# Optimization experiments

Measured on AMD Instinct MI355X. Metric: run time of the kernel, lower is better.

## Reference

```python
import jax, jax.numpy as jnp
import numpy as np

B, N, C_IN, C_OUT, NUM_TYPES = 4, 4096, 128, 64, 5
TEMP = 1.0  # self.temp is undefined in the source; use 1.0


def setup_inputs() -> dict:
    key = jax.random.key(0)
    ks = jax.random.split(key, 9)
    bound_p = np.sqrt(6.0 / (C_IN + C_OUT))
    bound_k = np.sqrt(6.0 / (C_OUT + 1))
    return {
        "node_rep": jax.random.normal(ks[0], (B, N, C_IN), dtype=jnp.float32),
        "adj_matrix": jax.random.uniform(ks[1], (N, N), dtype=jnp.float32),
        "node_type": jax.random.randint(ks[2], (N,), 0, NUM_TYPES),
        "proj_W": jax.random.uniform(ks[3], (C_OUT, C_IN), minval=-bound_p, maxval=bound_p, dtype=jnp.float32),
        "proj_b": jnp.zeros((C_OUT,), dtype=jnp.float32),
        "k_W": jax.random.uniform(ks[4], (NUM_TYPES, C_OUT), minval=-bound_k, maxval=bound_k, dtype=jnp.float32),
        "k_b": jnp.zeros((NUM_TYPES,), dtype=jnp.float32),
        "v_W": jax.random.uniform(ks[5], (NUM_TYPES, C_OUT), minval=-bound_k, maxval=bound_k, dtype=jnp.float32),
        "v_b": jnp.zeros((NUM_TYPES,), dtype=jnp.float32),
    }


def reference(node_rep, adj_matrix, node_type, proj_W, proj_b, k_W, k_b, v_W, v_b):
    # projection: [B,N,c_in] -> [B,N,c_out]
    h = jnp.einsum('bnc,oc->bno', node_rep, proj_W) + proj_b
    # per-type scalar scores stacked: [B,N,num_types]
    ks = jnp.einsum('bno,to->bnt', h, k_W) + k_b
    vs = jnp.einsum('bno,to->bnt', h, v_W) + v_b
    # gather score of each node's own type -> [B,N,1]
    idx = jnp.broadcast_to(node_type[None, :, None], (h.shape[0], h.shape[1], 1))
    f1 = jnp.take_along_axis(ks, idx, axis=2)           # [B,N,1]
    f2 = jnp.take_along_axis(vs, idx, axis=2)           # [B,N,1]
    # pairwise logits masked/weighted by adjacency: [B,N,N]
    attn_logits = adj_matrix[None, :, :] * (f1 + jnp.swapaxes(f2, 1, 2))
    unnorm = jax.nn.sigmoid(attn_logits) - 0.5
    attn_probs = jax.nn.softmax(unnorm / TEMP, axis=1)  # softmax over dim 1, as in source
    # aggregate: [B,N,N] @ [B,N,c_out] -> [B,N,c_out]
    return jnp.matmul(attn_probs, h)
```

## Files before the change

### kernel.cpp

```cpp
#include <hip/hip_runtime.h>
#include <hip/hip_bf16.h>
#include <stdint.h>

#define NN   4096
#define BB   4
#define CIN  128
#define COUT 64
#define JSPL 4
#define ITIL 32
#define NIT  (NN / ITIL)

typedef __attribute__((ext_vector_type(4))) float f32x4;
typedef __attribute__((ext_vector_type(8))) short s16x8;
typedef __attribute__((ext_vector_type(4))) int   i32x4;

__device__ __forceinline__ float sig_exp(float u) {
    const float L = 1.4426950408889634f;
    float e0 = __builtin_amdgcn_exp2f(-u * L);
    float sg = __builtin_amdgcn_rcpf(1.0f + e0);
    return __builtin_amdgcn_exp2f(__builtin_fmaf(sg, L, -0.7213475204444817f));
}

__device__ __forceinline__ short f2bf(float x) {
    unsigned u = __builtin_bit_cast(unsigned, x);
    return (short)((u + 0x8000u) >> 16);
}

__global__ __launch_bounds__(256) void k_proj(
    const float* __restrict__ node_rep, const int* __restrict__ node_type,
    const float* __restrict__ pW, const float* __restrict__ pb,
    const float* __restrict__ kW, const float* __restrict__ kb,
    const float* __restrict__ vW, const float* __restrict__ vb,
    float* __restrict__ h, float* __restrict__ f1, float* __restrict__ f2)
{
    int row = blockIdx.x * 4 + (threadIdx.x >> 6);
    int o   = threadIdx.x & 63;
    int n   = row & (NN - 1);

    const f32x4* xr = (const f32x4*)(node_rep + (size_t)row * CIN);
    const f32x4* wr = (const f32x4*)(pW + (size_t)o * CIN);
    float a0 = pb[o], a1 = 0.f, a2 = 0.f, a3 = 0.f;
    #pragma unroll
    for (int c = 0; c < CIN / 4; ++c) {
        f32x4 x = xr[c], w = wr[c];
        a0 = fmaf(x[0], w[0], a0);
        a1 = fmaf(x[1], w[1], a1);
        a2 = fmaf(x[2], w[2], a2);
        a3 = fmaf(x[3], w[3], a3);
    }
    float acc = (a0 + a1) + (a2 + a3);
    h[(size_t)row * COUT + o] = acc;

    int t = node_type[n];
    float s1 = acc * kW[t * COUT + o];
    float s2 = acc * vW[t * COUT + o];
    #pragma unroll
    for (int off = 32; off; off >>= 1) {
        s1 += __shfl_xor(s1, off, 64);
        s2 += __shfl_xor(s2, off, 64);
    }
    if (o == 0) { f1[row] = s1 + kb[t]; f2[row] = s2 + vb[t]; }
}

__global__ __launch_bounds__(256) void k_denom(
    const float* __restrict__ adj, const float* __restrict__ f1,
    const float* __restrict__ f2, float* __restrict__ pd)
{
    int j  = blockIdx.x * 256 + threadIdx.x;
    int it = blockIdx.y;
    int i0 = it * ITIL;
    float f2r[BB], acc[BB];
    #pragma unroll
    for (int b = 0; b < BB; ++b) { f2r[b] = f2[b * NN + j]; acc[b] = 0.0f; }
    #pragma unroll 2
    for (int ii = 0; ii < ITIL; ii += 2) {
        float a0 = adj[(size_t)(i0 + ii)     * NN + j];
        float a1 = adj[(size_t)(i0 + ii + 1) * NN + j];
        #pragma unroll
        for (int b = 0; b < BB; ++b) {
            float fa = f1[b * NN + i0 + ii];
            float fb = f1[b * NN + i0 + ii + 1];
            acc[b] += sig_exp(a0 * (fa + f2r[b])) + sig_exp(a1 * (fb + f2r[b]));
        }
    }
    #pragma unroll
    for (int b = 0; b < BB; ++b) pd[(size_t)(it * BB + b) * NN + j] = acc[b];
}

__global__ __launch_bounds__(256) void k_dred(
    const float* __restrict__ pd, float* __restrict__ rden)
{
    int gid = blockIdx.x * 256 + threadIdx.x;
    float s = 0.0f;
    for (int it = 0; it < NIT; ++it) s += pd[(size_t)it * BB * NN + gid];
    rden[gid] = 1.0f / s;
}

__global__ __launch_bounds__(256) void k_hst(
    const float* __restrict__ h, const float* __restrict__ rden,
    unsigned short* __restrict__ hsT)
{
    int b  = blockIdx.y;
    int j0 = blockIdx.x * 64;
    __shared__ float tile[64][65];
    int cx = threadIdx.x & 63;
    int ry = threadIdx.x >> 6;
    #pragma unroll
    for (int k = 0; k < 16; ++k) {
        int jl = k * 4 + ry;
        float d = rden[b * NN + j0 + jl];
        tile[jl][cx] = h[((size_t)b * NN + j0 + jl) * COUT + cx] * d;
    }
    __syncthreads();
    #pragma unroll
    for (int k = 0; k < 16; ++k) {
        int cl = k * 4 + ry;
        hsT[((size_t)b * COUT + cl) * NN + j0 + cx] = (unsigned short)f2bf(tile[cx][cl]);
    }
}

__global__ __launch_bounds__(512) void k_out(
    const float* __restrict__ adj, const float* __restrict__ f1,
    const float* __restrict__ f2, const unsigned short* __restrict__ hsT,
    float* __restrict__ pout)
{
    int i0   = blockIdx.x * 16;
    int jsp  = blockIdx.y;
    int tid  = threadIdx.x;
    int wid  = tid >> 6;
    int lane = tid & 63;
    int lrow = lane & 15;
    int lgrp = lane >> 4;

    const float* arow = adj + (size_t)(i0 + lrow) * NN;
    float f1v[BB];
    #pragma unroll
    for (int b = 0; b < BB; ++b) f1v[b] = f1[b * NN + i0 + lrow];

    f32x4 acc[BB][4];
    #pragma unroll
    for (int b = 0; b < BB; ++b)
        #pragma unroll
        for (int r = 0; r < 4; ++r) acc[b][r] = (f32x4){0.f, 0.f, 0.f, 0.f};

    int jbeg = jsp * (NN / JSPL) + wid * (NN / JSPL / 8);
    for (int js = 0; js < NN / JSPL / 8; js += 32) {
        int jk = jbeg + js + lgrp * 8;
        f32x4 a0 = *(const f32x4*)(arow + jk);
        f32x4 a1 = *(const f32x4*)(arow + jk + 4);

        #pragma unroll
        for (int b = 0; b < BB; ++b) {
            const float* f2b = f2 + b * NN;
            f32x4 s0 = *(const f32x4*)(f2b + jk);
            f32x4 s1 = *(const f32x4*)(f2b + jk + 4);

            float e[8];
            #pragma unroll
            for (int q = 0; q < 4; ++q) {
                e[q]     = sig_exp(a0[q] * (f1v[b] + s0[q]));
                e[q + 4] = sig_exp(a1[q] * (f1v[b] + s1[q]));
            }
            s16x8 af;
            #pragma unroll
            for (int q = 0; q < 8; ++q) af[q] = f2bf(e[q]);

            const unsigned short* hsb = hsT + (size_t)b * COUT * NN;
            s16x8 b0 = __builtin_bit_cast(s16x8, *(const i32x4*)(hsb + (size_t)(0  + lrow) * NN + jk));
            s16x8 b1 = __builtin_bit_cast(s16x8, *(const i32x4*)(hsb + (size_t)(16 + lrow) * NN + jk));
            s16x8 b2 = __builtin_bit_cast(s16x8, *(const i32x4*)(hsb + (size_t)(32 + lrow) * NN + jk));
            s16x8 b3 = __builtin_bit_cast(s16x8, *(const i32x4*)(hsb + (size_t)(48 + lrow) * NN + jk));

            acc[b][0] = __builtin_amdgcn_mfma_f32_16x16x32_bf16(af, b0, acc[b][0], 0, 0, 0);
            acc[b][1] = __builtin_amdgcn_mfma_f32_16x16x32_bf16(af, b1, acc[b][1], 0, 0, 0);
            acc[b][2] = __builtin_amdgcn_mfma_f32_16x16x32_bf16(af, b2, acc[b][2], 0, 0, 0);
            acc[b][3] = __builtin_amdgcn_mfma_f32_16x16x32_bf16(af, b3, acc[b][3], 0, 0, 0);
        }
    }

    __shared__ float red[8][16][64];
    #pragma unroll
    for (int b = 0; b < BB; ++b) {
        if (b) __syncthreads();
        #pragma unroll
        for (int r = 0; r < 4; ++r) {
            red[wid][lgrp * 4 + r][ 0 + lrow] = acc[b][0][r];
            red[wid][lgrp * 4 + r][16 + lrow] = acc[b][1][r];
            red[wid][lgrp * 4 + r][32 + lrow] = acc[b][2][r];
            red[wid][lgrp * 4 + r][48 + lrow] = acc[b][3][r];
        }
        __syncthreads();

        int e2 = tid * 2;
        int ii = e2 >> 6;
        int cc = e2 & 63;
        float sx = 0.f, sy = 0.f;
        #pragma unroll
        for (int w = 0; w < 8; ++w) {
            sx += red[w][ii][cc];
            sy += red[w][ii][cc + 1];
        }
        float* op = pout + ((size_t)(jsp * BB + b) * NN + i0 + ii) * COUT + cc;
        op[0] = sx; op[1] = sy;
    }
}

__global__ __launch_bounds__(256) void k_ored(
    const float* __restrict__ pout, float* __restrict__ out)
{
    size_t e = ((size_t)blockIdx.x * 256 + threadIdx.x) * 4;
    f32x4 s = *(const f32x4*)(pout + e);
    #pragma unroll
    for (int sp = 1; sp < JSPL; ++sp)
        s += *(const f32x4*)(pout + (size_t)sp * BB * NN * COUT + e);
    *(f32x4*)(out + e) = s;
}

extern "C" void kernel_launch(void* const* d_in, const int* in_sizes, int n_in,
                              void* d_out, int out_size, void* d_ws, size_t ws_size,
                              hipStream_t stream)
{
    const float* node_rep = (const float*)d_in[0];
    const float* adj      = (const float*)d_in[1];
    const int*   ntype    = (const int*)  d_in[2];
    const float* pW       = (const float*)d_in[3];
    const float* pb       = (const float*)d_in[4];
    const float* kW       = (const float*)d_in[5];
    const float* kb       = (const float*)d_in[6];
    const float* vW       = (const float*)d_in[7];
    const float* vb       = (const float*)d_in[8];
    float* out = (float*)d_out;

    char* w = (char*)d_ws;
    float*          h     = (float*)(w);
    float*          f1    = (float*)(w + 4194304);
    float*          f2    = (float*)(w + 4259840);
    float*          rden  = (float*)(w + 4325376);
    unsigned short* hsT   = (unsigned short*)(w + 4390912);
    float*          pd    = (float*)(w + 6488064);
    float*          pout  = (float*)(w + 14876672);

    k_proj <<<BB * NN / 4, 256, 0, stream>>>(node_rep, ntype, pW, pb, kW, kb, vW, vb, h, f1, f2);
    k_denom<<<dim3(NN / 256, NIT), 256, 0, stream>>>(adj, f1, f2, pd);
    k_dred <<<BB * NN / 256, 256, 0, stream>>>(pd, rden);
    k_hst  <<<dim3(NN / 64, BB), 256, 0, stream>>>(h, rden, hsT);
    k_out  <<<dim3(NN / 16, JSPL), 512, 0, stream>>>(adj, f1, f2, hsT, pout);
    k_ored <<<BB * NN * COUT / 1024, 256, 0, stream>>>(pout, out);
}
```

Measured before the change: 286.6 us.

## Fuse denominator reduction via atomics and restructure output kernel per-batch waves

After: 344.8 us. 1.2x slower.

```diff
diff --git a/kernel.cpp b/kernel.cpp
--- a/kernel.cpp
+++ b/kernel.cpp
@@ -7,8 +7,6 @@
 #define CIN  128
 #define COUT 64
 #define JSPL 4
-#define ITIL 32
-#define NIT  (NN / ITIL)
 
 typedef __attribute__((ext_vector_type(4))) float f32x4;
 typedef __attribute__((ext_vector_type(8))) short s16x8;
@@ -31,8 +29,12 @@
     const float* __restrict__ pW, const float* __restrict__ pb,
     const float* __restrict__ kW, const float* __restrict__ kb,
     const float* __restrict__ vW, const float* __restrict__ vb,
-    float* __restrict__ h, float* __restrict__ f1, float* __restrict__ f2)
-{
+    float* __restrict__ h, float* __restrict__ f1, float* __restrict__ f2,
+    float* __restrict__ denom)
+{
+    if (blockIdx.x < (BB * NN) / 256)
+        denom[blockIdx.x * 256 + threadIdx.x] = 0.0f;
+
     int row = blockIdx.x * 4 + (threadIdx.x >> 6);
     int o   = threadIdx.x & 63;
     int n   = row & (NN - 1);
@@ -64,40 +66,45 @@
 
 __global__ __launch_bounds__(256) void k_denom(
     const float* __restrict__ adj, const float* __restrict__ f1,
-    const float* __restrict__ f2, float* __restrict__ pd)
-{
-    int j  = blockIdx.x * 256 + threadIdx.x;
-    int it = blockIdx.y;
-    int i0 = it * ITIL;
-    float f2r[BB], acc[BB];
-    #pragma unroll
-    for (int b = 0; b < BB; ++b) { f2r[b] = f2[b * NN + j]; acc[b] = 0.0f; }
-    #pragma unroll 2
-    for (int ii = 0; ii < ITIL; ii += 2) {
-        float a0 = adj[(size_t)(i0 + ii)     * NN + j];
-        float a1 = adj[(size_t)(i0 + ii + 1) * NN + j];
+    const float* __restrict__ f2, float* __restrict__ denom)
+{
+    int j4 = blockIdx.x * 1024 + threadIdx.x * 4;
+    int i0 = blockIdx.y * 16;
+
+    f32x4 f2r[BB], acc[BB];
+    #pragma unroll
+    for (int b = 0; b < BB; ++b) {
+        f2r[b] = *(const f32x4*)(f2 + b * NN + j4);
+        acc[b] = (f32x4){0.f, 0.f, 0.f, 0.f};
+    }
+
+    const float* abase = adj + (size_t)i0 * NN + j4;
+    f32x4 aA = *(const f32x4*)(abase);
+    for (int ii = 0; ii < 16; ii += 2) {
+        f32x4 aB = *(const f32x4*)(abase + (size_t)(ii + 1) * NN);
         #pragma unroll
         for (int b = 0; b < BB; ++b) {
-            float fa = f1[b * NN + i0 + ii];
-            float fb = f1[b * NN + i0 + ii + 1];
-            acc[b] += sig_exp(a0 * (fa + f2r[b])) + sig_exp(a1 * (fb + f2r[b]));
+            float fv = f1[b * NN + i0 + ii];
+            #pragma unroll
+            for (int q = 0; q < 4; ++q) acc[b][q] += sig_exp(aA[q] * (fv + f2r[b][q]));
         }
-    }
-    #pragma unroll
-    for (int b = 0; b < BB; ++b) pd[(size_t)(it * BB + b) * NN + j] = acc[b];
-}
-
-__global__ __launch_bounds__(256) void k_dred(
-    const float* __restrict__ pd, float* __restrict__ rden)
-{
-    int gid = blockIdx.x * 256 + threadIdx.x;
-    float s = 0.0f;
-    for (int it = 0; it < NIT; ++it) s += pd[(size_t)it * BB * NN + gid];
-    rden[gid] = 1.0f / s;
+        if (ii + 2 < 16) aA = *(const f32x4*)(abase + (size_t)(ii + 2) * NN);
+        #pragma unroll
+        for (int b = 0; b < BB; ++b) {
+            float fv = f1[b * NN + i0 + ii + 1];
+            #pragma unroll
+            for (int q = 0; q < 4; ++q) acc[b][q] += sig_exp(aB[q] * (fv + f2r[b][q]));
+        }
+    }
+    #pragma unroll
+    for (int b = 0; b < BB; ++b)
+        #pragma unroll
+        for (int q = 0; q < 4; ++q)
+            atomicAdd(&denom[b * NN + j4 + q], acc[b][q]);
 }
 
 __global__ __launch_bounds__(256) void k_hst(
-    const float* __restrict__ h, const float* __restrict__ rden,
+    const float* __restrict__ h, const float* __restrict__ denom,
     unsigned short* __restrict__ hsT)
 {
     int b  = blockIdx.y;
@@ -108,8 +115,8 @@
     #pragma unroll
     for (int k = 0; k < 16; ++k) {
         int jl = k * 4 + ry;
-        float d = rden[b * NN + j0 + jl];
-        tile[jl][cx] = h[((size_t)b * NN + j0 + jl) * COUT + cx] * d;
+        float rd = __builtin_amdgcn_rcpf(denom[b * NN + j0 + jl]);
+        tile[jl][cx] = h[((size_t)b * NN + j0 + jl) * COUT + cx] * rd;
     }
     __syncthreads();
     #pragma unroll
@@ -119,89 +126,77 @@
     }
 }
 
-__global__ __launch_bounds__(512) void k_out(
+__global__ __launch_bounds__(256, 4) void k_out(
     const float* __restrict__ adj, const float* __restrict__ f1,
     const float* __restrict__ f2, const unsigned short* __restrict__ hsT,
     float* __restrict__ pout)
 {
     int i0   = blockIdx.x * 16;
     int jsp  = blockIdx.y;
-    int tid  = threadIdx.x;
-    int wid  = tid >> 6;
-    int lane = tid & 63;
+    int b    = threadIdx.x >> 6;
+    int lane = threadIdx.x & 63;
     int lrow = lane & 15;
     int lgrp = lane >> 4;
 
-    const float* arow = adj + (size_t)(i0 + lrow) * NN;
-    float f1v[BB];
-    #pragma unroll
-    for (int b = 0; b < BB; ++b) f1v[b] = f1[b * NN + i0 + lrow];
-
-    f32x4 acc[BB][4];
-    #pragma unroll
-    for (int b = 0; b < BB; ++b)
-        #pragma unroll
-        for (int r = 0; r < 4; ++r) acc[b][r] = (f32x4){0.f, 0.f, 0.f, 0.f};
-
-    int jbeg = jsp * (NN / JSPL) + wid * (NN / JSPL / 8);
-    for (int js = 0; js < NN / JSPL / 8; js += 32) {
-        int jk = jbeg + js + lgrp * 8;
-        f32x4 a0 = *(const f32x4*)(arow + jk);
-        f32x4 a1 = *(const f32x4*)(arow + jk + 4);
-
-        #pragma unroll
-        for (int b = 0; b < BB; ++b) {
-            const float* f2b = f2 + b * NN;
-            f32x4 s0 = *(const f32x4*)(f2b + jk);
-            f32x4 s1 = *(const f32x4*)(f2b + jk + 4);
-
-            float e[8];
-            #pragma unroll
-            for (int q = 0; q < 4; ++q) {
-                e[q]     = sig_exp(a0[q] * (f1v[b] + s0[q]));
-                e[q + 4] = sig_exp(a1[q] * (f1v[b] + s1[q]));
-            }
-            s16x8 af;
-            #pragma unroll
-            for (int q = 0; q < 8; ++q) af[q] = f2bf(e[q]);
-
-            const unsigned short* hsb = hsT + (size_t)b * COUT * NN;
-            s16x8 b0 = __builtin_bit_cast(s16x8, *(const i32x4*)(hsb + (size_t)(0  + lrow) * NN + jk));
-            s16x8 b1 = __builtin_bit_cast(s16x8, *(const i32x4*)(hsb + (size_t)(16 + lrow) * NN + jk));
-            s16x8 b2 = __builtin_bit_cast(s16x8, *(const i32x4*)(hsb + (size_t)(32 + lrow) * NN + jk));
-            s16x8 b3 = __builtin_bit_cast(s16x8, *(const i32x4*)(hsb + (size_t)(48 + lrow) * NN + jk));
-
-            acc[b][0] = __builtin_amdgcn_mfma_f32_16x16x32_bf16(af, b0, acc[b][0], 0, 0, 0);
-            acc[b][1] = __builtin_amdgcn_mfma_f32_16x16x32_bf16(af, b1, acc[b][1], 0, 0, 0);
-            acc[b][2] = __builtin_amdgcn_mfma_f32_16x16x32_bf16(af, b2, acc[b][2], 0, 0, 0);
-            acc[b][3] = __builtin_amdgcn_mfma_f32_16x16x32_bf16(af, b3, acc[b][3], 0, 0, 0);
-        }
-    }
-
-    __shared__ float red[8][16][64];
-    #pragma unroll
-    for (int b = 0; b < BB; ++b) {
-        if (b) __syncthreads();
-        #pragma unroll
-        for (int r = 0; r < 4; ++r) {
-            red[wid][lgrp * 4 + r][ 0 + lrow] = acc[b][0][r];
-            red[wid][lgrp * 4 + r][16 + lrow] = acc[b][1][r];
-            red[wid][lgrp * 4 + r][32 + lrow] = acc[b][2][r];
-            red[wid][lgrp * 4 + r][48 + lrow] = acc[b][3][r];
-        }
-        __syncthreads();
-
-        int e2 = tid * 2;
-        int ii = e2 >> 6;
-        int cc = e2 & 63;
-        float sx = 0.f, sy = 0.f;
-        #pragma unroll
-        for (int w = 0; w < 8; ++w) {
-            sx += red[w][ii][cc];
-            sy += red[w][ii][cc + 1];
-        }
-        float* op = pout + ((size_t)(jsp * BB + b) * NN + i0 + ii) * COUT + cc;
-        op[0] = sx; op[1] = sy;
+    const float*          arow = adj + (size_t)(i0 + lrow) * NN;
+    const float*          f2b  = f2 + b * NN;
+    const unsigned short* hsb  = hsT + ((size_t)b * COUT + lrow) * NN;
+    float f1v = f1[b * NN + i0 + lrow];
+
+    f32x4 acc0 = {0.f, 0.f, 0.f, 0.f};
+    f32x4 acc1 = acc0, acc2 = acc0, acc3 = acc0;
+
+    int jb = jsp * (NN / JSPL) + lgrp * 8;
+
+#define LDAH(t, a0, a1, h0, h1, h2, h3) {                                  \
+    int jk = jb + (t) * 32;                                                \
+    a0 = *(const f32x4*)(arow + jk);                                       \
+    a1 = *(const f32x4*)(arow + jk + 4);                                   \
+    h0 = *(const i32x4*)(hsb + jk);                                        \
+    h1 = *(const i32x4*)(hsb + (size_t)16 * NN + jk);                      \
+    h2 = *(const i32x4*)(hsb + (size_t)32 * NN + jk);                      \
+    h3 = *(const i32x4*)(hsb + (size_t)48 * NN + jk); }
+
+#define COMP(t, a0, a1, h0, h1, h2, h3) {                                  \
+    int jk = jb + (t) * 32;                                                \
+    f32x4 s0 = *(const f32x4*)(f2b + jk);                                  \
+    f32x4 s1 = *(const f32x4*)(f2b + jk + 4);                              \
+    float e0 = sig_exp(a0[0] * (f1v + s0[0]));                             \
+    float e1 = sig_exp(a0[1] * (f1v + s0[1]));                             \
+    float e2 = sig_exp(a0[2] * (f1v + s0[2]));                             \
+    float e3 = sig_exp(a0[3] * (f1v + s0[3]));                             \
+    float e4 = sig_exp(a1[0] * (f1v + s1[0]));                             \
+    float e5 = sig_exp(a1[1] * (f1v + s1[1]));                             \
+    float e6 = sig_exp(a1[2] * (f1v + s1[2]));                             \
+    float e7 = sig_exp(a1[3] * (f1v + s1[3]));                             \
+    s16x8 af;                                                              \
+    af[0] = f2bf(e0); af[1] = f2bf(e1); af[2] = f2bf(e2); af[3] = f2bf(e3);\
+    af[4] = f2bf(e4); af[5] = f2bf(e5); af[6] = f2bf(e6); af[7] = f2bf(e7);\
+    acc0 = __builtin_amdgcn_mfma_f32_16x16x32_bf16(af, __builtin_bit_cast(s16x8, h0), acc0, 0, 0, 0); \
+    acc1 = __builtin_amdgcn_mfma_f32_16x16x32_bf16(af, __builtin_bit_cast(s16x8, h1), acc1, 0, 0, 0); \
+    acc2 = __builtin_amdgcn_mfma_f32_16x16x32_bf16(af, __builtin_bit_cast(s16x8, h2), acc2, 0, 0, 0); \
+    acc3 = __builtin_amdgcn_mfma_f32_16x16x32_bf16(af, __builtin_bit_cast(s16x8, h3), acc3, 0, 0, 0); }
+
+    f32x4 Aa0, Aa1, Ba0, Ba1;
+    i32x4 Ah0, Ah1, Ah2, Ah3, Bh0, Bh1, Bh2, Bh3;
+    const int T = NN / JSPL / 32;
+    LDAH(0, Aa0, Aa1, Ah0, Ah1, Ah2, Ah3);
+    for (int t = 0; t < T; t += 2) {
+        LDAH(t + 1, Ba0, Ba1, Bh0, Bh1, Bh2, Bh3);
+        COMP(t, Aa0, Aa1, Ah0, Ah1, Ah2, Ah3);
+        if (t + 2 < T) LDAH(t + 2, Aa0, Aa1, Ah0, Ah1, Ah2, Ah3);
+        COMP(t + 1, Ba0, Ba1, Bh0, Bh1, Bh2, Bh3);
+    }
+#undef LDAH
+#undef COMP
+
+    #pragma unroll
+    for (int r = 0; r < 4; ++r) {
+        float* orow = pout + ((size_t)(jsp * BB + b) * NN + i0 + lgrp * 4 + r) * COUT + lrow;
+        orow[ 0] = acc0[r];
+        orow[16] = acc1[r];
+        orow[32] = acc2[r];
+        orow[48] = acc3[r];
     }
 }
 
@@ -235,15 +230,13 @@
     float*          h     = (float*)(w);
     float*          f1    = (float*)(w + 4194304);
     float*          f2    = (float*)(w + 4259840);
-    float*          rden  = (float*)(w + 4325376);
+    float*          denom = (float*)(w + 4325376);
     unsigned short* hsT   = (unsigned short*)(w + 4390912);
-    float*          pd    = (float*)(w + 6488064);
-    float*          pout  = (float*)(w + 14876672);
-
-    k_proj <<<BB * NN / 4, 256, 0, stream>>>(node_rep, ntype, pW, pb, kW, kb, vW, vb, h, f1, f2);
-    k_denom<<<dim3(NN / 256, NIT), 256, 0, stream>>>(adj, f1, f2, pd);
-    k_dred <<<BB * NN / 256, 256, 0, stream>>>(pd, rden);
-    k_hst  <<<dim3(NN / 64, BB), 256, 0, stream>>>(h, rden, hsT);
-    k_out  <<<dim3(NN / 16, JSPL), 512, 0, stream>>>(adj, f1, f2, hsT, pout);
+    float*          pout  = (float*)(w + 6488064);
+
+    k_proj <<<BB * NN / 4, 256, 0, stream>>>(node_rep, ntype, pW, pb, kW, kb, vW, vb, h, f1, f2, denom);
+    k_denom<<<dim3(NN / 1024, NN / 16), 256, 0, stream>>>(adj, f1, f2, denom);
+    k_hst  <<<dim3(NN / 64, BB), 256, 0, stream>>>(h, denom, hsT);
+    k_out  <<<dim3(NN / 16, JSPL), 256, 0, stream>>>(adj, f1, f2, hsT, pout);
     k_ored <<<BB * NN * COUT / 1024, 256, 0, stream>>>(pout, out);
 }
```
